# Performance work log

Measured on AMD Instinct MI355X. Metric: run time of the kernel, lower is better.

## Reference

```python
import jax, jax.numpy as jnp
from jax import lax
import numpy as np

# Constants from the source module
DMIN, DMAX = 1.0, 50.0
NUM_PLANES = 8            # number of depth-hypothesis planes
FOCAL = 307.98 // 4.0     # focal // downsample (stride-4 features) -> 76.0 px

B, C, H, W = 4, 64, 96, 320


def _plane_shifts(dtype):
    # reciprocal (inverse-depth) spaced hypothesis planes: d_i = 1/disp_i
    disp = jnp.linspace(1.0 / DMAX, 1.0 / DMIN, NUM_PLANES, dtype=dtype)
    return (FOCAL * disp).astype(dtype)  # per-plane vertical pixel shift f/d


def _warp_vertical(x, shifts):
    """Bilinear vertical homography warp of x [B,C,H,W] for each shift.
    Returns [B,D,C,H,W]; out-of-image samples are zero."""
    Bb, Cc, Hh, Ww = x.shape
    D = shifts.shape[0]
    y = jnp.arange(Hh, dtype=x.dtype)                 # [H]
    y_src = y[None, :] + shifts[:, None]              # [D,H]
    y0 = jnp.floor(y_src)
    w = (y_src - y0)                                  # bilinear weight [D,H]
    y0i = y0.astype(jnp.int32)
    y1i = y0i + 1
    v0 = ((y0i >= 0) & (y0i < Hh)).astype(x.dtype)    # validity masks [D,H]
    v1 = ((y1i >= 0) & (y1i < Hh)).astype(x.dtype)
    y0c = jnp.clip(y0i, 0, Hh - 1).reshape(-1)        # [D*H]
    y1c = jnp.clip(y1i, 0, Hh - 1).reshape(-1)
    # gather rows: [B,C,D*H,W] -> [B,C,D,H,W]
    g0 = jnp.take(x, y0c, axis=2).reshape(Bb, Cc, D, Hh, Ww)
    g1 = jnp.take(x, y1c, axis=2).reshape(Bb, Cc, D, Hh, Ww)
    wb = w[None, None, :, :, None]
    out = (1.0 - wb) * v0[None, None, :, :, None] * g0 + wb * v1[None, None, :, :, None] * g1
    return jnp.transpose(out, (0, 2, 1, 3, 4))        # [B,D,C,H,W]


def _depth_recip_conv(x, Wk, b):
    """Warp to each hypothesis plane, conv each, max-project over planes."""
    Bb, Cc, Hh, Ww = x.shape
    warped = _warp_vertical(x, _plane_shifts(x.dtype))        # [B,D,C,H,W]
    D = warped.shape[1]
    xr = warped.reshape(Bb * D, Cc, Hh, Ww)
    y = lax.conv_general_dilated(xr, Wk, window_strides=(1, 1), padding='SAME',
                                 dimension_numbers=('NCHW', 'OIHW', 'NCHW'))
    Co = Wk.shape[0]
    y = y.reshape(Bb, D, Co, Hh, Ww).max(axis=1)              # max-projection
    return y + b[None, :, None, None]


def setup_inputs() -> dict:
    key = jax.random.key(0)
    k1, k2, k3, k4, k5 = jax.random.split(key, 5)
    fan = C * 9
    return {
        'x': jax.random.normal(k1, (B, C, H, W), dtype=jnp.float32),
        'W1': jax.random.normal(k2, (C, C, 3, 3), dtype=jnp.float32) / np.sqrt(fan),
        'b1': jax.random.normal(k3, (C,), dtype=jnp.float32) * 0.01,
        'W2': jax.random.normal(k4, (C, C, 3, 3), dtype=jnp.float32) / np.sqrt(fan),
        'b2': jax.random.normal(k5, (C,), dtype=jnp.float32) * 0.01,
    }


def reference(x, W1, b1, W2, b2):
    x = jax.nn.relu(_depth_recip_conv(x, W1, b1))
    x = jax.nn.relu(_depth_recip_conv(x, W2, b2))
    return x
```

## Files before the change

kernel.cpp:

```cpp
#include <hip/hip_runtime.h>
#include <math.h>

#define HH 96
#define WW 320
#define NP 8

typedef _Float16 half8_t  __attribute__((ext_vector_type(8)));
typedef _Float16 half4_t  __attribute__((ext_vector_type(4)));
typedef float    floatx16 __attribute__((ext_vector_type(16)));

struct ShiftInfo {
    int   s0[NP];
    float wa[NP];
    float wb[NP];
    int   rows[16];
};

__device__ __forceinline__ void gl_lds16(const _Float16* g, _Float16* l) {
    __builtin_amdgcn_global_load_lds(
        (const __attribute__((address_space(1))) void*)g,
        (__attribute__((address_space(3))) void*)l, 16, 0, 0);
}

__global__ __launch_bounds__(256) void prep_kernel(
    const float* __restrict__ X, const float* __restrict__ W1,
    const float* __restrict__ W2, _Float16* __restrict__ Xt,
    _Float16* __restrict__ Wf)
{
    __shared__ __align__(16) _Float16 Ls[64 * 163];
    const int bx = blockIdx.x, t = threadIdx.x;
    if (bx < 768) {
        const int r = bx >> 1, xh = bx & 1;
        const int y = r % HH, b = r / HH;
        const int xbase = xh * 160;
        for (int u = t; u < 64 * 40; u += 256) {
            int ci = u / 40;
            int xi = (u - ci * 40) * 4;
            float4 v = *(const float4*)&X[((size_t)(b * 64 + ci) * HH + y) * WW + xbase + xi];
            half4_t hv = { (_Float16)v.x, (_Float16)v.y, (_Float16)v.z, (_Float16)v.w };
            *(half4_t*)&Ls[ci * 163 + xi] = hv;
        }
        __syncthreads();
        const int ci8 = t & 7, xg = t >> 3;
        for (int it = 0; it < 5; ++it) {
            int x = xg + 32 * it;
            half8_t o;
#pragma unroll
            for (int j = 0; j < 8; ++j) o[j] = Ls[(ci8 * 8 + j) * 163 + x];
            *(half8_t*)&Xt[((size_t)(b * HH + y) * WW + xbase + x) * 64 + ci8 * 8] = o;
        }
    } else {
        const int k = bx - 768;
        const int layer = k / 9, pos = k - layer * 9;
        const float* Ws = layer ? W2 : W1;
        _Float16* Wd = Wf + layer * 36864 + pos * 4096;
        for (int u = t; u < 4096; u += 256) {
            int mt  = u >> 11;
            int ks  = (u >> 9) & 3;
            int i31 = (u >> 4) & 31;
            int h   = (u >> 3) & 1;
            int j   = u & 7;
            int co  = mt * 32 + i31;
            int ci  = ks * 16 + h * 8 + j;
            Wd[u] = (_Float16)Ws[((size_t)co * 64 + ci) * 9 + pos];
        }
    }
}

template<int MODE, int NPOS>
__device__ __forceinline__ void conv_core(
    const _Float16* __restrict__ Xs, int w, int i31, int h,
    const _Float16* wp0, floatx16 (&acc)[2][2])
{
    constexpr int NI = NPOS * 4;
    half8_t fw0[4], fw1[4], fx0[4], fx1[4];

    int xsw[3], xbase[3];
#pragma unroll
    for (int kx = 0; kx < 3; ++kx) {
        int x = i31 + kx;
        xsw[kx]   = x & 7;
        xbase[kx] = x * 64;
    }
    const int rowb = w * (66 * 64);

    auto ld = [&](int idx, int s) {
        const int pos = idx >> 2, ks = idx & 3;
        const int ky = pos / 3, kx = pos - ky * 3;
        const _Float16* wp = wp0 + pos * 4096 + ks * 512;
        fw0[s] = *(const half8_t*)(wp);
        fw1[s] = *(const half8_t*)(wp + 2048);
        const int c8  = ks * 2 + h;
        const int off = rowb + ky * (66 * 64) + xbase[kx] + ((c8 ^ xsw[kx]) * 8);
        fx0[s] = *(const half8_t*)(Xs + off);
        fx1[s] = *(const half8_t*)(Xs + off + 32 * 64);
    };

#pragma unroll
    for (int s = 0; s < 3; ++s) ld(s, s);

#pragma unroll
    for (int i = 0; i < NI; ++i) {
        if (i + 3 < NI) ld(i + 3, (i + 3) & 3);
        const int s = i & 3;
        if (MODE == 1) {
            acc[0][0] = __builtin_amdgcn_mfma_f32_32x32x16_f16(fx0[s], fw0[s], acc[0][0], 0, 0, 0);
            acc[0][1] = __builtin_amdgcn_mfma_f32_32x32x16_f16(fx0[s], fw1[s], acc[0][1], 0, 0, 0);
            acc[1][0] = __builtin_amdgcn_mfma_f32_32x32x16_f16(fx1[s], fw0[s], acc[1][0], 0, 0, 0);
            acc[1][1] = __builtin_amdgcn_mfma_f32_32x32x16_f16(fx1[s], fw1[s], acc[1][1], 0, 0, 0);
        } else {
            acc[0][0] = __builtin_amdgcn_mfma_f32_32x32x16_f16(fw0[s], fx0[s], acc[0][0], 0, 0, 0);
            acc[0][1] = __builtin_amdgcn_mfma_f32_32x32x16_f16(fw0[s], fx1[s], acc[0][1], 0, 0, 0);
            acc[1][0] = __builtin_amdgcn_mfma_f32_32x32x16_f16(fw1[s], fx0[s], acc[1][0], 0, 0, 0);
            acc[1][1] = __builtin_amdgcn_mfma_f32_32x32x16_f16(fw1[s], fx1[s], acc[1][1], 0, 0, 0);
        }
    }
}

template<int MODE>
__global__ __launch_bounds__(256, 3) void conv_kernel(
    const _Float16* __restrict__ Xt, const _Float16* __restrict__ Wfl,
    _Float16* __restrict__ OutE, _Float16* __restrict__ OutT, ShiftInfo si)
{
    __shared__ __align__(16) _Float16 Xs[6 * 66 * 64];
    const int xt = blockIdx.x, rg = blockIdx.y, b = blockIdx.z;
    const bool top = rg >= 24;
    const int trg = rg - 24;
    const int x0 = xt * 64;
    const int t  = threadIdx.x;

    int grow[6];
#pragma unroll
    for (int r = 0; r < 6; ++r)
        grow[r] = top ? ((r < 4) ? si.rows[trg * 4 + r] : -1) : rg * 4 + r;

    {
        const int w = t >> 6, l = t & 63;
#pragma unroll
        for (int j = 0; j < 12; ++j) {
            int k = w + 4 * j;
            int r = k >> 3, c = k & 7;
            if ((unsigned)grow[r] < HH) {
                int x  = 1 + 8 * c + (l >> 3);
                int c8 = (l & 7) ^ (x & 7);
                const _Float16* g =
                    &Xt[((size_t)(b * HH + grow[r]) * WW + (x0 - 1 + x)) * 64 + c8 * 8];
                gl_lds16(g, &Xs[(r * 66 + 1 + 8 * c) * 64]);
            }
        }
    }

#pragma unroll
    for (int r = 0; r < 6; ++r) {
        if ((unsigned)grow[r] >= HH) {
            for (int u = t; u < 66 * 8; u += 256) {
                float4 zz = make_float4(0.f, 0.f, 0.f, 0.f);
                *(float4*)&Xs[r * (66 * 64) + u * 8] = zz;
            }
        }
    }

    if (t < 96) {
        int r  = t >> 4, hx = (t >> 3) & 1, c8 = t & 7;
        int x  = hx ? 65 : 0;
        int gx = x0 - 1 + x;
        float4 v = make_float4(0.f, 0.f, 0.f, 0.f);
        if ((unsigned)grow[r] < HH && (unsigned)gx < WW)
            v = *(const float4*)&Xt[((size_t)(b * HH + grow[r]) * WW + gx) * 64 + c8 * 8];
        *(float4*)&Xs[(r * 66 + x) * 64 + ((c8 ^ (x & 7)) * 8)] = v;
    }
    __syncthreads();

    const int l = t & 63, w = t >> 6;
    const int i31 = l & 31, h = l >> 5;

    floatx16 acc[2][2];
#pragma unroll
    for (int a = 0; a < 2; ++a)
#pragma unroll
        for (int c = 0; c < 2; ++c)
            acc[a][c] = (floatx16){0.f,0.f,0.f,0.f, 0.f,0.f,0.f,0.f,
                                   0.f,0.f,0.f,0.f, 0.f,0.f,0.f,0.f};

    const _Float16* wp0 = Wfl + i31 * 16 + h * 8;
    if (top) conv_core<MODE, 3>(Xs, w, i31, h, wp0, acc);
    else     conv_core<MODE, 9>(Xs, w, i31, h, wp0, acc);

    const int OH = top ? 16 : HH;
    const int om = top ? (trg * 4 + w) : (rg * 4 + w);
    _Float16* Out = top ? OutT : OutE;
#pragma unroll
    for (int a = 0; a < 2; ++a)
#pragma unroll
        for (int c = 0; c < 2; ++c)
#pragma unroll
            for (int r = 0; r < 16; ++r) {
                int dm = (r & 3) + 8 * (r >> 2) + 4 * h;
                if (MODE == 1) {
                    int x  = x0 + a * 32 + dm;
                    int co = c * 32 + i31;
                    Out[((size_t)(b * OH + om) * WW + x) * 64 + co] = (_Float16)acc[a][c][r];
                } else {
                    int co = a * 32 + dm;
                    int x  = x0 + c * 32 + i31;
                    Out[((size_t)(b * 64 + co) * OH + om) * WW + x] = (_Float16)acc[a][c][r];
                }
            }
}

__global__ __launch_bounds__(256) void blend1_kernel(
    const _Float16* __restrict__ Cb, const _Float16* __restrict__ T,
    const float* __restrict__ bias, _Float16* __restrict__ Xt2, ShiftInfo si)
{
    __shared__ __align__(16) _Float16 Cs[96 * 64];
    __shared__ __align__(16) _Float16 Ts[16 * 64];
    const int x0 = blockIdx.x, b = blockIdx.y, t = threadIdx.x;
    const half8_t z = {0,0,0,0,0,0,0,0};

    {
        const int w = t >> 6, l = t & 63;
        const int c8 = l & 7;
#pragma unroll
        for (int j = 0; j < 3; ++j) {
            int k = w + 4 * j;
            int row = 8 * k + (l >> 3);
            gl_lds16(&Cb[((size_t)(b * HH + row) * WW + x0) * 64 + c8 * 8],
                     &Cs[k * 512]);
        }
        if (w < 2) {
            int row = 8 * w + (l >> 3);
            gl_lds16(&T[((size_t)(b * 16 + row) * WW + x0) * 64 + c8 * 8],
                     &Ts[w * 512]);
        }
    }
    __syncthreads();

    const int co8 = t & 7, yt = t >> 3;
    half8_t bv;
#pragma unroll
    for (int j = 0; j < 8; ++j) bv[j] = (_Float16)bias[co8 * 8 + j];

    const int y0 = yt * 3;
    half8_t cur[NP];
#pragma unroll
    for (int d = 0; d < NP; ++d) {
        int r = y0 + si.s0[d] - 1;
        cur[d] = (r < HH) ? *(const half8_t*)&Cs[r * 64 + co8 * 8] : z;
    }
    for (int y = y0; y < y0 + 3; ++y) {
        half8_t m = z;
#pragma unroll
        for (int d = 0; d < NP; ++d) {
            int r1 = y + si.s0[d];
            half8_t v1 = (r1 < HH) ? *(const half8_t*)&Cs[r1 * 64 + co8 * 8] : z;
            half8_t v0 = cur[d];
            cur[d] = v1;
            _Float16 a = (_Float16)si.wa[d], wg = (_Float16)si.wb[d];
            half8_t p;
            if (y == 0) {
                half8_t t0 = *(const half8_t*)&Ts[(2 * d) * 64 + co8 * 8];
                half8_t t1 = *(const half8_t*)&Ts[(2 * d + 1) * 64 + co8 * 8];
                p = a * (v0 - t0) + wg * (v1 - t1);
            } else {
                p = a * v0 + wg * v1;
            }
            m = (d == 0) ? p : __builtin_elementwise_max(m, p);
        }
        half8_t o = __builtin_elementwise_max(m + bv, z);
        *(half8_t*)&Xt2[((size_t)(b * HH + y) * WW + x0) * 64 + co8 * 8] = o;
    }
}

__global__ __launch_bounds__(256) void blend2_kernel(
    const _Float16* __restrict__ Cb, const _Float16* __restrict__ T,
    const float* __restrict__ bias, float* __restrict__ Out, ShiftInfo si)
{
    __shared__ __align__(16) _Float16 Cs[96 * 64];
    __shared__ __align__(16) _Float16 Ts[16 * 64];
    const int task = blockIdx.x, t = threadIdx.x;
    const int xt = task % 5;
    const int rem = task / 5;
    const int co = rem & 63;
    const int b  = rem >> 6;
    const int x0 = xt * 64;
    const half8_t z = {0,0,0,0,0,0,0,0};

    {
        const int w = t >> 6, l = t & 63;
        const int x8 = l & 7;
#pragma unroll
        for (int j = 0; j < 3; ++j) {
            int k = w + 4 * j;
            int row = 8 * k + (l >> 3);
            gl_lds16(&Cb[((size_t)(b * 64 + co) * HH + row) * WW + x0 + x8 * 8],
                     &Cs[k * 512]);
        }
        if (w < 2) {
            int row = 8 * w + (l >> 3);
            gl_lds16(&T[((size_t)(b * 64 + co) * 16 + row) * WW + x0 + x8 * 8],
                     &Ts[w * 512]);
        }
    }
    __syncthreads();

    const int x8 = t & 7, yt = t >> 3;
    const float bvf = bias[co];
    const int y0 = yt * 3;

    half8_t cur[NP];
#pragma unroll
    for (int d = 0; d < NP; ++d) {
        int r = y0 + si.s0[d] - 1;
        cur[d] = (r < HH) ? *(const half8_t*)&Cs[r * 64 + x8 * 8] : z;
    }
    for (int y = y0; y < y0 + 3; ++y) {
        half8_t m = z;
#pragma unroll
        for (int d = 0; d < NP; ++d) {
            int r1 = y + si.s0[d];
            half8_t v1 = (r1 < HH) ? *(const half8_t*)&Cs[r1 * 64 + x8 * 8] : z;
            half8_t v0 = cur[d];
            cur[d] = v1;
            _Float16 a = (_Float16)si.wa[d], wg = (_Float16)si.wb[d];
            half8_t p;
            if (y == 0) {
                half8_t t0 = *(const half8_t*)&Ts[(2 * d) * 64 + x8 * 8];
                half8_t t1 = *(const half8_t*)&Ts[(2 * d + 1) * 64 + x8 * 8];
                p = a * (v0 - t0) + wg * (v1 - t1);
            } else {
                p = a * v0 + wg * v1;
            }
            m = (d == 0) ? p : __builtin_elementwise_max(m, p);
        }
        float4 o0, o1;
        o0.x = fmaxf((float)m[0] + bvf, 0.f);
        o0.y = fmaxf((float)m[1] + bvf, 0.f);
        o0.z = fmaxf((float)m[2] + bvf, 0.f);
        o0.w = fmaxf((float)m[3] + bvf, 0.f);
        o1.x = fmaxf((float)m[4] + bvf, 0.f);
        o1.y = fmaxf((float)m[5] + bvf, 0.f);
        o1.z = fmaxf((float)m[6] + bvf, 0.f);
        o1.w = fmaxf((float)m[7] + bvf, 0.f);
        float* op = Out + ((size_t)(b * 64 + co) * HH + y) * WW + x0 + x8 * 8;
        *(float4*)op = o0;
        *(float4*)(op + 4) = o1;
    }
}

extern "C" void kernel_launch(void* const* d_in, const int* in_sizes, int n_in,
                              void* d_out, int out_size, void* d_ws, size_t ws_size,
                              hipStream_t stream) {
    const float* x  = (const float*)d_in[0];
    const float* W1 = (const float*)d_in[1];
    const float* b1 = (const float*)d_in[2];
    const float* W2 = (const float*)d_in[3];
    const float* b2 = (const float*)d_in[4];
    float* out = (float*)d_out;

    _Float16* Xt1 = (_Float16*)d_ws;
    _Float16* Cb  = Xt1 + 7864320;
    _Float16* T   = Cb  + 7864320;
    _Float16* Wf  = T   + 1310720;
    _Float16* Xt2 = (_Float16*)d_out;

    ShiftInfo si;
    for (int d = 0; d < NP; ++d) {
        double disp = 0.02 + d * (0.98 / 7.0);
        double sh   = 76.0 * disp;
        int s0      = (int)floor(sh);
        double w    = sh - (double)s0;
        si.s0[d] = s0;
        si.wa[d] = (float)(1.0 - w);
        si.wb[d] = (float)w;
        si.rows[2 * d]     = s0 - 1;
        si.rows[2 * d + 1] = s0;
    }

    prep_kernel<<<dim3(786), 256, 0, stream>>>(x, W1, W2, Xt1, Wf);

    conv_kernel<1><<<dim3(5, 28, 4), 256, 0, stream>>>(Xt1, Wf, Cb, T, si);
    blend1_kernel<<<dim3(320, 4), 256, 0, stream>>>(Cb, T, b1, Xt2, si);

    conv_kernel<2><<<dim3(5, 28, 4), 256, 0, stream>>>(Xt2, Wf + 36864, Cb, T, si);
    blend2_kernel<<<dim3(1280), 256, 0, stream>>>(Cb, T, b2, out, si);
}
```

Measured before the change: 78.55 us.

## Stage conv weights in double-buffered LDS via async global-to-LDS loads

Weight fragments, previously read per-wave straight from global memory inside the MFMA loop, are now copied per kernel position into a double-buffered LDS tile with global_load_lds. The next position's tile is prefetched while the current one is consumed, with a block barrier after each position. The register-level 3-deep software pipeline is replaced by a load-all-four-then-compute block per position. LDS use grows by 16 KB and occupancy bounds drop from 3 to 2 blocks per SM. The per-position barriers may add stalls.

```diff
diff --git a/kernel.cpp b/kernel.cpp
--- a/kernel.cpp
+++ b/kernel.cpp
@@ -69,12 +69,10 @@
 
 template<int MODE, int NPOS>
 __device__ __forceinline__ void conv_core(
-    const _Float16* __restrict__ Xs, int w, int i31, int h,
-    const _Float16* wp0, floatx16 (&acc)[2][2])
+    const _Float16* __restrict__ Xs, _Float16* __restrict__ Wl,
+    const _Float16* __restrict__ Wg, int w, int i31, int h, int t,
+    floatx16 (&acc)[2][2])
 {
-    constexpr int NI = NPOS * 4;
-    half8_t fw0[4], fw1[4], fx0[4], fx1[4];
-
     int xsw[3], xbase[3];
 #pragma unroll
     for (int kx = 0; kx < 3; ++kx) {
@@ -82,47 +80,57 @@
         xsw[kx]   = x & 7;
         xbase[kx] = x * 64;
     }
-    const int rowb = w * (66 * 64);
-
-    auto ld = [&](int idx, int s) {
-        const int pos = idx >> 2, ks = idx & 3;
-        const int ky = pos / 3, kx = pos - ky * 3;
-        const _Float16* wp = wp0 + pos * 4096 + ks * 512;
-        fw0[s] = *(const half8_t*)(wp);
-        fw1[s] = *(const half8_t*)(wp + 2048);
-        const int c8  = ks * 2 + h;
-        const int off = rowb + ky * (66 * 64) + xbase[kx] + ((c8 ^ xsw[kx]) * 8);
-        fx0[s] = *(const half8_t*)(Xs + off);
-        fx1[s] = *(const half8_t*)(Xs + off + 32 * 64);
-    };
-
-#pragma unroll
-    for (int s = 0; s < 3; ++s) ld(s, s);
-
-#pragma unroll
-    for (int i = 0; i < NI; ++i) {
-        if (i + 3 < NI) ld(i + 3, (i + 3) & 3);
-        const int s = i & 3;
-        if (MODE == 1) {
-            acc[0][0] = __builtin_amdgcn_mfma_f32_32x32x16_f16(fx0[s], fw0[s], acc[0][0], 0, 0, 0);
-            acc[0][1] = __builtin_amdgcn_mfma_f32_32x32x16_f16(fx0[s], fw1[s], acc[0][1], 0, 0, 0);
-            acc[1][0] = __builtin_amdgcn_mfma_f32_32x32x16_f16(fx1[s], fw0[s], acc[1][0], 0, 0, 0);
-            acc[1][1] = __builtin_amdgcn_mfma_f32_32x32x16_f16(fx1[s], fw1[s], acc[1][1], 0, 0, 0);
-        } else {
-            acc[0][0] = __builtin_amdgcn_mfma_f32_32x32x16_f16(fw0[s], fx0[s], acc[0][0], 0, 0, 0);
-            acc[0][1] = __builtin_amdgcn_mfma_f32_32x32x16_f16(fw0[s], fx1[s], acc[0][1], 0, 0, 0);
-            acc[1][0] = __builtin_amdgcn_mfma_f32_32x32x16_f16(fw1[s], fx0[s], acc[1][0], 0, 0, 0);
-            acc[1][1] = __builtin_amdgcn_mfma_f32_32x32x16_f16(fw1[s], fx1[s], acc[1][1], 0, 0, 0);
-        }
+    const int rowb  = w * (66 * 64);
+    const int wv    = t >> 6, l = t & 63;
+    const int wfrag = i31 * 16 + h * 8;
+
+#pragma unroll
+    for (int p = 0; p < NPOS; ++p) {
+        if (p + 1 < NPOS) {
+#pragma unroll
+            for (int j = 0; j < 2; ++j) {
+                int ch = wv * 2 + j;
+                gl_lds16(Wg + (p + 1) * 4096 + ch * 512 + l * 8,
+                         Wl + ((p + 1) & 1) * 4096 + ch * 512);
+            }
+        }
+        const int ky = p / 3, kx = p - ky * 3;
+        const _Float16* wb = Wl + (p & 1) * 4096 + wfrag;
+        half8_t fw0[4], fw1[4], fx0[4], fx1[4];
+#pragma unroll
+        for (int ks = 0; ks < 4; ++ks) {
+            fw0[ks] = *(const half8_t*)(wb + ks * 512);
+            fw1[ks] = *(const half8_t*)(wb + ks * 512 + 2048);
+            const int c8  = ks * 2 + h;
+            const int off = rowb + ky * (66 * 64) + xbase[kx] + ((c8 ^ xsw[kx]) * 8);
+            fx0[ks] = *(const half8_t*)(Xs + off);
+            fx1[ks] = *(const half8_t*)(Xs + off + 32 * 64);
+        }
+#pragma unroll
+        for (int ks = 0; ks < 4; ++ks) {
+            if (MODE == 1) {
+                acc[0][0] = __builtin_amdgcn_mfma_f32_32x32x16_f16(fx0[ks], fw0[ks], acc[0][0], 0, 0, 0);
+                acc[0][1] = __builtin_amdgcn_mfma_f32_32x32x16_f16(fx0[ks], fw1[ks], acc[0][1], 0, 0, 0);
+                acc[1][0] = __builtin_amdgcn_mfma_f32_32x32x16_f16(fx1[ks], fw0[ks], acc[1][0], 0, 0, 0);
+                acc[1][1] = __builtin_amdgcn_mfma_f32_32x32x16_f16(fx1[ks], fw1[ks], acc[1][1], 0, 0, 0);
+            } else {
+                acc[0][0] = __builtin_amdgcn_mfma_f32_32x32x16_f16(fw0[ks], fx0[ks], acc[0][0], 0, 0, 0);
+                acc[0][1] = __builtin_amdgcn_mfma_f32_32x32x16_f16(fw0[ks], fx1[ks], acc[0][1], 0, 0, 0);
+                acc[1][0] = __builtin_amdgcn_mfma_f32_32x32x16_f16(fw1[ks], fx0[ks], acc[1][0], 0, 0, 0);
+                acc[1][1] = __builtin_amdgcn_mfma_f32_32x32x16_f16(fw1[ks], fx1[ks], acc[1][1], 0, 0, 0);
+            }
+        }
+        if (p + 1 < NPOS) __syncthreads();
     }
 }
 
 template<int MODE>
-__global__ __launch_bounds__(256, 3) void conv_kernel(
+__global__ __launch_bounds__(256, 2) void conv_kernel(
     const _Float16* __restrict__ Xt, const _Float16* __restrict__ Wfl,
     _Float16* __restrict__ OutE, _Float16* __restrict__ OutT, ShiftInfo si)
 {
     __shared__ __align__(16) _Float16 Xs[6 * 66 * 64];
+    __shared__ __align__(16) _Float16 Wl[2 * 4096];
     const int xt = blockIdx.x, rg = blockIdx.y, b = blockIdx.z;
     const bool top = rg >= 24;
     const int trg = rg - 24;
@@ -133,6 +141,15 @@
 #pragma unroll
     for (int r = 0; r < 6; ++r)
         grow[r] = top ? ((r < 4) ? si.rows[trg * 4 + r] : -1) : rg * 4 + r;
+
+    {
+        const int wv = t >> 6, l = t & 63;
+#pragma unroll
+        for (int j = 0; j < 2; ++j) {
+            int ch = wv * 2 + j;
+            gl_lds16(Wfl + ch * 512 + l * 8, Wl + ch * 512);
+        }
+    }
 
     {
         const int w = t >> 6, l = t & 63;
@@ -182,9 +199,8 @@
             acc[a][c] = (floatx16){0.f,0.f,0.f,0.f, 0.f,0.f,0.f,0.f,
                                    0.f,0.f,0.f,0.f, 0.f,0.f,0.f,0.f};
 
-    const _Float16* wp0 = Wfl + i31 * 16 + h * 8;
-    if (top) conv_core<MODE, 3>(Xs, w, i31, h, wp0, acc);
-    else     conv_core<MODE, 9>(Xs, w, i31, h, wp0, acc);
+    if (top) conv_core<MODE, 3>(Xs, Wl, Wfl, w, i31, h, t, acc);
+    else     conv_core<MODE, 9>(Xs, Wl, Wfl, w, i31, h, t, acc);
 
     const int OH = top ? 16 : HH;
     const int om = top ? (trg * 4 + w) : (rg * 4 + w);
```

After: 77.44 us. No clear change (-1.4%).
